# Performance work log

Hardware: AMD Instinct MI355X
Metric: run time of the kernel (lower is better)

Reference implementation:

```python
import jax, jax.numpy as jnp
import numpy as np
from jax import lax

EPS = 1e-5

def conv2d(x, w, pad, dil):
    # x: NCHW, w: OIHW
    return lax.conv_general_dilated(
        x, w, window_strides=(1, 1), padding=[(pad, pad), (pad, pad)],
        rhs_dilation=(dil, dil), dimension_numbers=("NCHW", "OIHW", "NCHW"))

def batchnorm(x, gamma, beta):
    # training-mode BN: batch statistics over (N, H, W), biased variance
    m = x.mean(axis=(0, 2, 3), keepdims=True)
    v = x.var(axis=(0, 2, 3), keepdims=True)
    xh = (x - m) * lax.rsqrt(v + EPS)
    return gamma[None, :, None, None] * xh + beta[None, :, None, None]

def maxpool2(x):
    return lax.reduce_window(x, -jnp.inf, lax.max, (1, 1, 2, 2), (1, 1, 2, 2), "VALID")

def mhsa(x, wq, bq, wk, bk, wv, bv, rel_h, rel_w, heads=1):
    B, C, H, W = x.shape
    N = H * W
    d = C // heads
    q = (conv2d(x, wq, 0, 1) + bq[None, :, None, None]).reshape(B, heads, d, N)
    k = (conv2d(x, wk, 0, 1) + bk[None, :, None, None]).reshape(B, heads, d, N)
    v = (conv2d(x, wv, 0, 1) + bv[None, :, None, None]).reshape(B, heads, d, N)
    # content-content: q^T k -> [B, h, N, N]
    cc = jnp.einsum("bhdn,bhdm->bhnm", q, k)
    # content-position: (rel_h + rel_w) reshaped to [h, d, N], transposed, times q
    pos = (rel_h + rel_w).reshape(heads, d, N)  # broadcast-sum [1,h,d,1,H]+[1,h,d,W,1]
    cp = jnp.einsum("hnd,bhdm->bhnm", jnp.swapaxes(pos, 1, 2), q)
    attn = jax.nn.softmax(cc + cp, axis=-1)
    # out = v @ attn^T
    out = jnp.einsum("bhdn,bhmn->bhdm", v, attn)
    return out.reshape(B, C, H, W)


def setup_inputs() -> dict:
    key = jax.random.key(0)
    ks = jax.random.split(key, 16)
    B, in_ch, out_ch, S = 4, 128, 256, 64
    c4 = out_ch // 4  # 64 = MHSA channel dim
    w_scale = 0.05
    inp = {
        "x": jax.random.normal(ks[0], (B, in_ch, 2 * S, 2 * S), jnp.float32),
        "dc_w1": jax.random.normal(ks[1], (out_ch, in_ch, 3, 3), jnp.float32) * w_scale,
        "dc_b1": jnp.zeros((out_ch,), jnp.float32),
        "dc_g1": jnp.ones((out_ch,), jnp.float32),
        "dc_be1": jnp.zeros((out_ch,), jnp.float32),
        "dc_w2": jax.random.normal(ks[2], (out_ch, out_ch, 3, 3), jnp.float32) * w_scale,
        "dc_b2": jnp.zeros((out_ch,), jnp.float32),
        "dc_g2": jnp.ones((out_ch,), jnp.float32),
        "dc_be2": jnp.zeros((out_ch,), jnp.float32),
        "aspp1_w": jax.random.normal(ks[3], (c4, out_ch, 1, 1), jnp.float32) * w_scale,
        "aspp1_g": jnp.ones((c4,), jnp.float32),
        "aspp1_b": jnp.zeros((c4,), jnp.float32),
        "aspp2_w": jax.random.normal(ks[4], (c4, out_ch, 3, 3), jnp.float32) * w_scale,
        "aspp2_g": jnp.ones((c4,), jnp.float32),
        "aspp2_b": jnp.zeros((c4,), jnp.float32),
        "aspp3_w": jax.random.normal(ks[5], (c4, out_ch, 3, 3), jnp.float32) * w_scale,
        "aspp3_g": jnp.ones((c4,), jnp.float32),
        "aspp3_b": jnp.zeros((c4,), jnp.float32),
        "aspp4_w": jax.random.normal(ks[6], (c4, out_ch, 3, 3), jnp.float32) * w_scale,
        "aspp4_g": jnp.ones((c4,), jnp.float32),
        "aspp4_b": jnp.zeros((c4,), jnp.float32),
        "wq": jax.random.normal(ks[7], (c4, c4, 1, 1), jnp.float32) * w_scale,
        "bq": jnp.zeros((c4,), jnp.float32),
        "wk": jax.random.normal(ks[8], (c4, c4, 1, 1), jnp.float32) * w_scale,
        "bk": jnp.zeros((c4,), jnp.float32),
        "wv": jax.random.normal(ks[9], (c4, c4, 1, 1), jnp.float32) * w_scale,
        "bv": jnp.zeros((c4,), jnp.float32),
        "rel_h": jax.random.normal(ks[10], (1, 1, c4, 1, S), jnp.float32),
        "rel_w": jax.random.normal(ks[11], (1, 1, c4, S, 1), jnp.float32),
    }
    return inp


def reference(x, dc_w1, dc_b1, dc_g1, dc_be1, dc_w2, dc_b2, dc_g2, dc_be2,
              aspp1_w, aspp1_g, aspp1_b, aspp2_w, aspp2_g, aspp2_b,
              aspp3_w, aspp3_g, aspp3_b, aspp4_w, aspp4_g, aspp4_b,
              wq, bq, wk, bk, wv, bv, rel_h, rel_w):
    dilations = (1, 3, 6, 9)
    # mpconv: MaxPool2d(2) -> double_conv
    h = maxpool2(x)
    h = jax.nn.relu(batchnorm(conv2d(h, dc_w1, 1, 1) + dc_b1[None, :, None, None], dc_g1, dc_be1))
    h = jax.nn.relu(batchnorm(conv2d(h, dc_w2, 1, 1) + dc_b2[None, :, None, None], dc_g2, dc_be2))

    aspp = [(aspp1_w, aspp1_g, aspp1_b), (aspp2_w, aspp2_g, aspp2_b),
            (aspp3_w, aspp3_g, aspp3_b), (aspp4_w, aspp4_g, aspp4_b)]
    outs = []
    for (w, g, b), dil in zip(aspp, dilations):
        pad = 0 if dil == 1 else dil
        branch = jax.nn.relu(batchnorm(conv2d(h, w, pad, dil), g, b))
        outs.append(mhsa(branch, wq, bq, wk, bk, wv, bv, rel_h, rel_w))
    return jnp.concatenate(outs, axis=1)
```

## Files before the change

### kernel.cpp

```cpp
#include <hip/hip_runtime.h>
#include <math.h>

constexpr int Bn = 4;
constexpr int S  = 64;
constexpr int N  = 4096;

#define DEV static __device__ __forceinline__

typedef __attribute__((ext_vector_type(8))) short bf16x8;
typedef __attribute__((ext_vector_type(4))) float f32x4;

DEV unsigned short bfc(float x) {
  unsigned u = __float_as_uint(x);
  unsigned r = (u + 0x7FFFu + ((u >> 16) & 1u)) >> 16;
  return (unsigned short)r;
}

DEV void fma4(float4& a, float s, const float4 u) {
  a.x = fmaf(s, u.x, a.x); a.y = fmaf(s, u.y, a.y);
  a.z = fmaf(s, u.z, a.z); a.w = fmaf(s, u.w, a.w);
}

DEV void gload_lds16(const unsigned short* g, unsigned short* l) {
  __builtin_amdgcn_global_load_lds(
      (const __attribute__((address_space(1))) void*)g,
      (__attribute__((address_space(3))) void*)l, 16, 0, 0);
}

DEV unsigned cvtpk_bf16(float lo, float hi) {
  unsigned r;
  asm("v_cvt_pk_bf16_f32 %0, %1, %2" : "=v"(r) : "v"(lo), "v"(hi));
  return r;
}
DEV void pswap32(unsigned& a, unsigned& b) {
  asm("v_permlane32_swap_b32 %0, %1" : "+v"(a), "+v"(b));
}
DEV void pswap16(unsigned& a, unsigned& b) {
  asm("v_permlane16_swap_b32 %0, %1" : "+v"(a), "+v"(b));
}

__global__ __launch_bounds__(256) void wtr_all_kernel(
    const float* __restrict__ w1, const float* __restrict__ w2,
    const float* __restrict__ a0, const float* __restrict__ a1,
    const float* __restrict__ a2, const float* __restrict__ a3,
    unsigned short* __restrict__ wt1, unsigned short* __restrict__ wt2,
    unsigned short* __restrict__ wtbr) {
  const int blk = blockIdx.x;
  const float* src; unsigned short* dst; int Cin, Cout, T, base;
  if (blk < 1152)      { src = w1; dst = wt1; Cout = 256; Cin = 128; T = 9; base = 0; }
  else if (blk < 3456) { src = w2; dst = wt2; Cout = 256; Cin = 256; T = 9; base = 1152; }
  else if (blk < 3520) { src = a0; dst = wtbr + (size_t)4 * 64 * 256;
                         Cout = 64; Cin = 256; T = 1; base = 3456; }
  else if (blk < 4096) { src = a1; dst = wtbr + (size_t)1 * 9 * 64 * 256;
                         Cout = 64; Cin = 256; T = 9; base = 3520; }
  else if (blk < 4672) { src = a2; dst = wtbr + (size_t)2 * 9 * 64 * 256;
                         Cout = 64; Cin = 256; T = 9; base = 4096; }
  else                 { src = a3; dst = wtbr + (size_t)3 * 9 * 64 * 256;
                         Cout = 64; Cin = 256; T = 9; base = 4672; }
  int i = (blk - base) * 256 + threadIdx.x;
  int ci = i % Cin;
  int r  = i / Cin;
  int t  = r / Cout;
  int co = r - t * Cout;
  dst[i] = bfc(src[((size_t)co * Cin + ci) * T + t]);
}

__global__ __launch_bounds__(256) void pool_kernel(const float* __restrict__ x,
                                                   unsigned short* __restrict__ Pp1) {
  int i = blockIdx.x * 256 + threadIdx.x;
  int xg = i & 15, y = (i >> 4) & 63, c = (i >> 10) & 127, b = i >> 17;
  const float* s = x + (((size_t)(b * 128 + c) * 128) + 2 * y) * 128 + 8 * xg;
  float4 u0 = *(const float4*)(s), u1 = *(const float4*)(s + 4);
  float4 u2 = *(const float4*)(s + 128), u3 = *(const float4*)(s + 132);
  float m0 = fmaxf(fmaxf(u0.x, u0.y), fmaxf(u2.x, u2.y));
  float m1 = fmaxf(fmaxf(u0.z, u0.w), fmaxf(u2.z, u2.w));
  float m2 = fmaxf(fmaxf(u1.x, u1.y), fmaxf(u3.x, u3.y));
  float m3 = fmaxf(fmaxf(u1.z, u1.w), fmaxf(u3.z, u3.w));
  unsigned short* d = Pp1 + (((size_t)b * 66 + y + 1) * 66 + xg * 4 + 1) * 128 + c;
  d[0] = bfc(m0); d[128] = bfc(m1); d[256] = bfc(m2); d[384] = bfc(m3);
}

template <int CTOT>
__global__ __launch_bounds__(256) void dcconv_kernel(
    const unsigned short* __restrict__ in, const unsigned short* __restrict__ wt,
    float* __restrict__ out) {
  const int Wp = 66, CSEG = CTOT / 2;
  const int w = threadIdx.x >> 6, lane = threadIdx.x & 63;
  const int ln = lane & 15, quad = lane >> 4;
  const int b = blockIdx.z >> 1, h = blockIdx.z & 1, co0 = blockIdx.y * 64;
  const int n0 = blockIdx.x * 128 + w * 32;
  const unsigned short* inb = in + (size_t)b * Wp * Wp * CTOT + h * CSEG;
  const unsigned short* wth = wt + h * CSEG;
  float* outh = out + (size_t)h * 4 * 256 * N;
  size_t pix[2];
#pragma unroll
  for (int j = 0; j < 2; j++) {
    int n = n0 + j * 16 + ln;
    int y = n >> 6, x = n & 63;
    pix[j] = ((size_t)y * Wp + x) * CTOT;
  }
  f32x4 acc[4][2];
#pragma unroll
  for (int i = 0; i < 4; i++)
#pragma unroll
    for (int j = 0; j < 2; j++) acc[i][j] = (f32x4)(0.f);
#pragma unroll
  for (int ky = 0; ky < 3; ky++)
#pragma unroll
    for (int kx = 0; kx < 3; kx++) {
      const size_t toff = ((size_t)ky * Wp + kx) * CTOT;
      const unsigned short* wtap = wth + (size_t)(ky * 3 + kx) * 256 * CTOT;
      for (int kc = 0; kc < CSEG / 32; kc++) {
        const int ko = kc * 32 + quad * 8;
        bf16x8 a[4], bb[2];
#pragma unroll
        for (int i = 0; i < 4; i++)
          a[i] = *(const bf16x8*)(wtap + (size_t)(co0 + i * 16 + ln) * CTOT + ko);
#pragma unroll
        for (int j = 0; j < 2; j++)
          bb[j] = *(const bf16x8*)(inb + pix[j] + toff + ko);
#pragma unroll
        for (int i = 0; i < 4; i++)
#pragma unroll
          for (int j = 0; j < 2; j++)
            acc[i][j] = __builtin_amdgcn_mfma_f32_16x16x32_bf16(a[i], bb[j], acc[i][j], 0, 0, 0);
      }
    }
#pragma unroll
  for (int i = 0; i < 4; i++)
#pragma unroll
    for (int j = 0; j < 2; j++)
#pragma unroll
      for (int r = 0; r < 4; r++)
        outh[((size_t)(b * 256 + co0 + i * 16 + quad * 4 + r)) * N + n0 + j * 16 + ln] =
            acc[i][j][r];
}

__global__ __launch_bounds__(256) void branch_kernel(
    const unsigned short* __restrict__ in, const unsigned short* __restrict__ wtall,
    float* __restrict__ br) {
  const int Wp = 82, halo = 9, CIN = 256;
  const int w = threadIdx.x >> 6, lane = threadIdx.x & 63;
  const int ln = lane & 15, quad = lane >> 4;
  const int bb = blockIdx.y;
  const int kbr = bb >> 2, b = bb & 3;
  const int dil = (kbr == 0) ? 1 : 3 * kbr;
  const int klo = (kbr == 0) ? 1 : 0, khi = (kbr == 0) ? 2 : 3;
  const int hd = halo - dil;
  const int cw = (w & 1) * 32, nw = (w >> 1) * 32;
  const int n0 = blockIdx.x * 64 + nw;
  const unsigned short* inb = in + (size_t)b * Wp * Wp * CIN;
  size_t pix[2];
#pragma unroll
  for (int j = 0; j < 2; j++) {
    int n = n0 + j * 16 + ln;
    int y = n >> 6, x = n & 63;
    pix[j] = ((size_t)(y + hd) * Wp + x + hd) * CIN;
  }
  f32x4 acc[2][2];
#pragma unroll
  for (int i = 0; i < 2; i++)
#pragma unroll
    for (int j = 0; j < 2; j++) acc[i][j] = (f32x4)(0.f);
  for (int ky = klo; ky < khi; ky++)
    for (int kx = klo; kx < khi; kx++) {
      const size_t toff = ((size_t)ky * Wp + kx) * dil * CIN;
      const unsigned short* wtap =
          wtall + ((size_t)kbr * 9 + ky * 3 + kx) * 64 * CIN;
      for (int kc = 0; kc < CIN / 32; kc++) {
        const int ko = kc * 32 + quad * 8;
        bf16x8 a[2], bv[2];
#pragma unroll
        for (int i = 0; i < 2; i++)
          a[i] = *(const bf16x8*)(wtap + (size_t)(cw + i * 16 + ln) * CIN + ko);
#pragma unroll
        for (int j = 0; j < 2; j++)
          bv[j] = *(const bf16x8*)(inb + pix[j] + toff + ko);
#pragma unroll
        for (int i = 0; i < 2; i++)
#pragma unroll
          for (int j = 0; j < 2; j++)
            acc[i][j] = __builtin_amdgcn_mfma_f32_16x16x32_bf16(a[i], bv[j], acc[i][j], 0, 0, 0);
      }
    }
#pragma unroll
  for (int i = 0; i < 2; i++)
#pragma unroll
    for (int j = 0; j < 2; j++)
#pragma unroll
      for (int r = 0; r < 4; r++)
        br[((size_t)bb * 64 + cw + i * 16 + quad * 4 + r) * N + n0 + j * 16 + ln] =
            acc[i][j][r];
}

__global__ __launch_bounds__(256) void bn_stats_all_kernel(
    const float* __restrict__ br,
    const float* __restrict__ g0, const float* __restrict__ b0,
    const float* __restrict__ g1, const float* __restrict__ b1,
    const float* __restrict__ g2, const float* __restrict__ b2,
    const float* __restrict__ g3, const float* __restrict__ b3,
    float* __restrict__ sta) {
  const int kbr = blockIdx.x >> 6, c = blockIdx.x & 63;
  const float* gamma = kbr == 0 ? g0 : (kbr == 1 ? g1 : (kbr == 2 ? g2 : g3));
  const float* beta  = kbr == 0 ? b0 : (kbr == 1 ? b1 : (kbr == 2 ? b2 : b3));
  const float* t = br + (size_t)kbr * 1048576;
  float* ss = sta + kbr * 128;
  float s = 0.f, s2 = 0.f;
  for (int b = 0; b < Bn; b++) {
    const float* p = t + ((size_t)(b * 64 + c)) * N;
    for (int i = threadIdx.x; i < N / 4; i += 256) {
      float4 v = *(const float4*)(p + (size_t)i * 4);
      s += (v.x + v.y) + (v.z + v.w);
      s2 = fmaf(v.x, v.x, s2); s2 = fmaf(v.y, v.y, s2);
      s2 = fmaf(v.z, v.z, s2); s2 = fmaf(v.w, v.w, s2);
    }
  }
  for (int off = 32; off; off >>= 1) {
    s += __shfl_down(s, off, 64);
    s2 += __shfl_down(s2, off, 64);
  }
  __shared__ float rs[4], rs2[4];
  const int wid = threadIdx.x >> 6, lane = threadIdx.x & 63;
  if (lane == 0) { rs[wid] = s; rs2[wid] = s2; }
  __syncthreads();
  if (threadIdx.x == 0) {
    float S1 = rs[0] + rs[1] + rs[2] + rs[3];
    float S2 = rs2[0] + rs2[1] + rs2[2] + rs2[3];
    const float cnt = (float)(Bn * N);
    float mean = S1 / cnt;
    float var = S2 / cnt - mean * mean;
    float sc = gamma[c] * rsqrtf(var + 1e-5f);
    ss[2 * c] = sc;
    ss[2 * c + 1] = beta[c] - mean * sc;
  }
}

__global__ __launch_bounds__(256) void bn_stats2_kernel(
    const float* __restrict__ ta, const float* __restrict__ tb,
    const float* __restrict__ gamma, const float* __restrict__ beta,
    float* __restrict__ ss, int C) {
  const int c = blockIdx.x;
  float s = 0.f, s2 = 0.f;
  for (int b = 0; b < Bn; b++) {
    const size_t base = ((size_t)(b * C + c)) * N;
    for (int i = threadIdx.x; i < N / 4; i += 256) {
      float4 va = *(const float4*)(ta + base + (size_t)i * 4);
      float4 vb = *(const float4*)(tb + base + (size_t)i * 4);
      float v0 = va.x + vb.x, v1 = va.y + vb.y;
      float v2 = va.z + vb.z, v3 = va.w + vb.w;
      s += (v0 + v1) + (v2 + v3);
      s2 = fmaf(v0, v0, s2); s2 = fmaf(v1, v1, s2);
      s2 = fmaf(v2, v2, s2); s2 = fmaf(v3, v3, s2);
    }
  }
  for (int off = 32; off; off >>= 1) {
    s += __shfl_down(s, off, 64);
    s2 += __shfl_down(s2, off, 64);
  }
  __shared__ float rs[4], rs2[4];
  const int wid = threadIdx.x >> 6, lane = threadIdx.x & 63;
  if (lane == 0) { rs[wid] = s; rs2[wid] = s2; }
  __syncthreads();
  if (threadIdx.x == 0) {
    float S1 = rs[0] + rs[1] + rs[2] + rs[3];
    float S2 = rs2[0] + rs2[1] + rs2[2] + rs2[3];
    const float cnt = (float)(Bn * N);
    float mean = S1 / cnt;
    float var = S2 / cnt - mean * mean;
    float sc = gamma[c] * rsqrtf(var + 1e-5f);
    ss[2 * c] = sc;
    ss[2 * c + 1] = beta[c] - mean * sc;
  }
}

__global__ __launch_bounds__(256) void bn_norm_pad2_kernel(
    const float* __restrict__ ta, const float* __restrict__ tb,
    const float* __restrict__ ss, unsigned short* __restrict__ outp,
    int Wp, int halo) {
  int i = blockIdx.x * 256 + threadIdx.x;
  int n = i & 4095, cg = (i >> 12) & 63, b = i >> 18;
  int c0 = cg * 4;
  ushort4 pk;
  float v0, v1, v2, v3;
  {
    size_t i0 = ((size_t)(b * 256 + c0 + 0)) * N + n;
    size_t i1 = i0 + N, i2 = i1 + N, i3 = i2 + N;
    v0 = fmaxf(fmaf(ta[i0] + tb[i0], ss[2 * (c0 + 0)], ss[2 * (c0 + 0) + 1]), 0.f);
    v1 = fmaxf(fmaf(ta[i1] + tb[i1], ss[2 * (c0 + 1)], ss[2 * (c0 + 1) + 1]), 0.f);
    v2 = fmaxf(fmaf(ta[i2] + tb[i2], ss[2 * (c0 + 2)], ss[2 * (c0 + 2) + 1]), 0.f);
    v3 = fmaxf(fmaf(ta[i3] + tb[i3], ss[2 * (c0 + 3)], ss[2 * (c0 + 3) + 1]), 0.f);
  }
  pk.x = bfc(v0); pk.y = bfc(v1); pk.z = bfc(v2); pk.w = bfc(v3);
  int y = n >> 6, x = n & 63;
  *(ushort4*)(outp + (((size_t)b * Wp + y + halo) * Wp + x + halo) * 256 + c0) = pk;
}

__global__ __launch_bounds__(256) void qkv_kernel(
    const float* __restrict__ br, const float* __restrict__ sta,
    const float* __restrict__ wq, const float* __restrict__ bq,
    const float* __restrict__ wk, const float* __restrict__ bk,
    const float* __restrict__ wv, const float* __restrict__ bvb,
    unsigned short* __restrict__ qTo, unsigned short* __restrict__ kTo,
    unsigned short* __restrict__ vbo) {
  const int bb = blockIdx.z;
  const int p = blockIdx.y >> 2, dg = blockIdx.y & 3;
  const float* w  = p == 0 ? wq : (p == 1 ? wk : wv);
  const float* bi = p == 0 ? bq : (p == 1 ? bk : bvb);
  __shared__ float wl[64 * 16];
  __shared__ float ssl[128];
  const int d0b = dg * 16;
  if (threadIdx.x < 128) ssl[threadIdx.x] = sta[(bb >> 2) * 128 + threadIdx.x];
  for (int i = threadIdx.x; i < 64 * 16; i += 256)
    wl[i] = w[(size_t)(d0b + (i & 15)) * 64 + (i >> 4)];
  __syncthreads();
  const int tn = threadIdx.x & 63, td = threadIdx.x >> 6;
  const int n0 = blockIdx.x * 256 + tn * 4;
  const int d0 = d0b + td * 4;
  const float* inb = br + (size_t)bb * 64 * N;
  float4 acc[4];
#pragma unroll
  for (int j = 0; j < 4; j++) {
    float bvv = bi[d0 + j];
    acc[j] = make_float4(bvv, bvv, bvv, bvv);
  }
  for (int ci = 0; ci < 64; ci++) {
    float4 u = *(const float4*)(inb + (size_t)ci * N + n0);
    const float sc = ssl[2 * ci], of = ssl[2 * ci + 1];
    u.x = fmaxf(fmaf(u.x, sc, of), 0.f);
    u.y = fmaxf(fmaf(u.y, sc, of), 0.f);
    u.z = fmaxf(fmaf(u.z, sc, of), 0.f);
    u.w = fmaxf(fmaf(u.w, sc, of), 0.f);
    float4 wv4 = *(const float4*)(wl + ci * 16 + td * 4);
    fma4(acc[0], wv4.x, u); fma4(acc[1], wv4.y, u);
    fma4(acc[2], wv4.z, u); fma4(acc[3], wv4.w, u);
  }
  const size_t slab = (size_t)bb * N * 64;
  if (p < 2) {
    unsigned short* o = (p == 0 ? qTo : kTo) + slab;
#pragma unroll
    for (int nn = 0; nn < 4; nn++) {
      ushort4 pk;
      pk.x = bfc(((const float*)&acc[0])[nn]);
      pk.y = bfc(((const float*)&acc[1])[nn]);
      pk.z = bfc(((const float*)&acc[2])[nn]);
      pk.w = bfc(((const float*)&acc[3])[nn]);
      *(ushort4*)(o + (size_t)(n0 + nn) * 64 + d0) = pk;
    }
  } else {
    unsigned short* o = vbo + slab;
#pragma unroll
    for (int j = 0; j < 4; j++) {
      ushort4 pk;
      pk.x = bfc(acc[j].x); pk.y = bfc(acc[j].y);
      pk.z = bfc(acc[j].z); pk.w = bfc(acc[j].w);
      *(ushort4*)(o + (size_t)(d0 + j) * N + n0) = pk;
    }
  }
}

__global__ __launch_bounds__(256) void posT_kernel(
    const float* __restrict__ rel_h, const float* __restrict__ rel_w,
    unsigned short* __restrict__ posT) {
  int i = blockIdx.x * 256 + threadIdx.x;
  int n = i >> 4, dq = (i & 15) * 4;
  int h = n >> 6, wc = n & 63;
  ushort4 pk;
  pk.x = bfc(rel_w[(dq + 0) * 64 + h] + rel_h[(dq + 0) * 64 + wc]);
  pk.y = bfc(rel_w[(dq + 1) * 64 + h] + rel_h[(dq + 1) * 64 + wc]);
  pk.z = bfc(rel_w[(dq + 2) * 64 + h] + rel_h[(dq + 2) * 64 + wc]);
  pk.w = bfc(rel_w[(dq + 3) * 64 + h] + rel_h[(dq + 3) * 64 + wc]);
  *(ushort4*)(posT + (size_t)n * 64 + dq) = pk;
}

__global__ __launch_bounds__(256, 3) void flash3_kernel(
    const unsigned short* __restrict__ qT, const unsigned short* __restrict__ kT,
    const unsigned short* __restrict__ posT, const unsigned short* __restrict__ vb,
    float* __restrict__ o_part, float* __restrict__ ml) {
  const int lin = blockIdx.x;
  const int xcd = lin & 7, slot = lin >> 3;
  const int bb = xcd * 2 + (slot & 1);
  const int rest = slot >> 1;
  const int mtile = rest & 31, split = rest >> 5;
  const size_t slab = (size_t)bb * N * 64;
  const unsigned short* qTs = qT + slab;
  const unsigned short* kTs = kT + slab;
  const unsigned short* vbs = vb + slab;
  const int w = threadIdx.x >> 6, lane = threadIdx.x & 63;
  const int ln = lane & 15, quad = lane >> 4;
  const int m0 = mtile * 128 + w * 32;
  __shared__ __align__(16) unsigned short As[2][4][64][32];

  const unsigned short* ssrc = (w < 2) ? kTs : qTs;
  const int rsub = lane >> 2;
  const int csw  = (lane & 3) ^ ((lane >> 3) & 3);
  const int ksub = (w & 1) * 32 + csw * 8;
  auto stage = [&](int c0, int bufi) {
#pragma unroll
    for (int j = 0; j < 4; j++)
      gload_lds16(ssrc + (size_t)(c0 + j * 16 + rsub) * 64 + ksub,
                  &As[bufi][w][j * 16][0]);
  };

  bf16x8 bq[4][2];
#pragma unroll
  for (int s = 0; s < 4; s++) {
    const unsigned short* src = (s < 2) ? qTs : posT;
#pragma unroll
    for (int mf = 0; mf < 2; mf++)
      bq[s][mf] = *(const bf16x8*)(src + (size_t)(m0 + mf * 16 + ln) * 64 +
                                   (s & 1) * 32 + quad * 8);
  }

  float m_run[2] = {-3.0e38f, -3.0e38f}, l_run[2] = {0.f, 0.f};
  f32x4 o_acc[4][2];
#pragma unroll
  for (int dt = 0; dt < 4; dt++)
#pragma unroll
    for (int mf = 0; mf < 2; mf++) o_acc[dt][mf] = (f32x4)(0.f);

  const int qsw = (quad ^ ((ln >> 1) & 3)) * 8;
  const int cbeg = split * 1024;
  stage(cbeg, 0);
  for (int t = 0; t < 16; t++) {
    const int c0 = cbeg + t * 64;
    const int buf = t & 1;
    __syncthreads();
    if (t < 15) stage(c0 + 64, buf ^ 1);
    f32x4 st[4][2];
#pragma unroll
    for (int jt = 0; jt < 4; jt++)
#pragma unroll
      for (int mf = 0; mf < 2; mf++) st[jt][mf] = (f32x4)(0.f);
    __builtin_amdgcn_s_setprio(1);
#pragma unroll
    for (int s = 0; s < 4; s++) {
#pragma unroll
      for (int jt = 0; jt < 4; jt++) {
        bf16x8 a = *(const bf16x8*)(&As[buf][s][jt * 16 + ln][qsw]);
#pragma unroll
        for (int mf = 0; mf < 2; mf++)
          st[jt][mf] = __builtin_amdgcn_mfma_f32_16x16x32_bf16(a, bq[s][mf], st[jt][mf], 0, 0, 0);
      }
    }
    __builtin_amdgcn_s_setprio(0);
    bf16x8 av[2][4];
#pragma unroll
    for (int tt = 0; tt < 2; tt++)
#pragma unroll
      for (int dt = 0; dt < 4; dt++)
        av[tt][dt] = *(const bf16x8*)(vbs + (size_t)(dt * 16 + ln) * N + c0 + tt * 32 + quad * 8);
    unsigned P0[2][4], P1[2][4];
#pragma unroll
    for (int mf = 0; mf < 2; mf++) {
      float mj[4];
#pragma unroll
      for (int jt = 0; jt < 4; jt++)
        mj[jt] = fmaxf(fmaxf(st[jt][mf][0], st[jt][mf][1]),
                       fmaxf(st[jt][mf][2], st[jt][mf][3]));
      float mx = fmaxf(fmaxf(mj[0], mj[1]), fmaxf(mj[2], mj[3]));
      mx = fmaxf(mx, __shfl_xor(mx, 16, 64));
      mx = fmaxf(mx, __shfl_xor(mx, 32, 64));
      if (!__all(mx <= m_run[mf])) {
        const float m_new = fmaxf(m_run[mf], mx);
        const float alpha = __expf(m_run[mf] - m_new);
        l_run[mf] *= alpha;
#pragma unroll
        for (int dt = 0; dt < 4; dt++)
#pragma unroll
          for (int r = 0; r < 4; r++) o_acc[dt][mf][r] *= alpha;
        m_run[mf] = m_new;
      }
      const float mc = m_run[mf];
      float psum = 0.f;
#pragma unroll
      for (int jt = 0; jt < 4; jt++) {
        float e0 = __expf(st[jt][mf][0] - mc);
        float e1 = __expf(st[jt][mf][1] - mc);
        float e2 = __expf(st[jt][mf][2] - mc);
        float e3 = __expf(st[jt][mf][3] - mc);
        psum += (e0 + e1) + (e2 + e3);
        P0[mf][jt] = cvtpk_bf16(e0, e1);
        P1[mf][jt] = cvtpk_bf16(e2, e3);
      }
      psum += __shfl_xor(psum, 16, 64);
      psum += __shfl_xor(psum, 32, 64);
      l_run[mf] += psum;
    }
    __builtin_amdgcn_s_setprio(1);
#pragma unroll
    for (int tt = 0; tt < 2; tt++) {
#pragma unroll
      for (int mf = 0; mf < 2; mf++) {
        unsigned x0 = P0[mf][2 * tt], y0 = P0[mf][2 * tt + 1];
        pswap32(x0, y0); pswap16(x0, y0);
        unsigned x1 = P1[mf][2 * tt], y1 = P1[mf][2 * tt + 1];
        pswap32(x1, y1); pswap16(x1, y1);
        union { unsigned u[4]; bf16x8 v; } bp;
        bp.u[0] = x0; bp.u[1] = x1; bp.u[2] = y0; bp.u[3] = y1;
#pragma unroll
        for (int dt = 0; dt < 4; dt++)
          o_acc[dt][mf] = __builtin_amdgcn_mfma_f32_16x16x32_bf16(av[tt][dt], bp.v, o_acc[dt][mf], 0, 0, 0);
      }
    }
    __builtin_amdgcn_s_setprio(0);
  }
  float* ob = o_part + ((size_t)(split * 16 + bb) * 64) * N;
#pragma unroll
  for (int dt = 0; dt < 4; dt++)
#pragma unroll
    for (int mf = 0; mf < 2; mf++)
#pragma unroll
      for (int r = 0; r < 4; r++) {
        int d = dt * 16 + quad * 4 + r;
        ob[(size_t)d * N + m0 + mf * 16 + ln] = o_acc[dt][mf][r];
      }
  if (quad == 0) {
#pragma unroll
    for (int mf = 0; mf < 2; mf++) {
      int m = m0 + mf * 16 + ln;
      ml[((size_t)(split * 16 + bb) * 2 + 0) * N + m] = m_run[mf];
      ml[((size_t)(split * 16 + bb) * 2 + 1) * N + m] = l_run[mf];
    }
  }
}

__global__ __launch_bounds__(256) void wcomb_kernel(const float* __restrict__ ml,
                                                    float* __restrict__ wcb) {
  int i = blockIdx.x * 256 + threadIdx.x;
  int m = i & 4095, bb = i >> 12;
  float mv[4], lv[4];
#pragma unroll
  for (int s = 0; s < 4; s++) {
    mv[s] = ml[((size_t)(s * 16 + bb) * 2 + 0) * N + m];
    lv[s] = ml[((size_t)(s * 16 + bb) * 2 + 1) * N + m];
  }
  float M = fmaxf(fmaxf(mv[0], mv[1]), fmaxf(mv[2], mv[3]));
  float wsc[4], denom = 0.f;
#pragma unroll
  for (int s = 0; s < 4; s++) {
    wsc[s] = __expf(mv[s] - M);
    denom = fmaf(wsc[s], lv[s], denom);
  }
  float inv = 1.0f / denom;
#pragma unroll
  for (int s = 0; s < 4; s++)
    wcb[(size_t)(s * 16 + bb) * N + m] = wsc[s] * inv;
}

__global__ __launch_bounds__(256) void comb_kernel(const float* __restrict__ o_part,
                                                   const float* __restrict__ wcb,
                                                   float* __restrict__ out) {
  int i = blockIdx.x * 256 + threadIdx.x;
  int m4 = i & 1023, d = (i >> 10) & 63, bb = i >> 16;
  int kbr = bb >> 2, b = bb & 3;
  float4 acc = make_float4(0.f, 0.f, 0.f, 0.f);
#pragma unroll
  for (int s = 0; s < 4; s++) {
    const float4 o = *(const float4*)(o_part + ((size_t)(s * 16 + bb) * 64 + d) * N + m4 * 4);
    const float4 wv = *(const float4*)(wcb + (size_t)(s * 16 + bb) * N + m4 * 4);
    acc.x = fmaf(o.x, wv.x, acc.x); acc.y = fmaf(o.y, wv.y, acc.y);
    acc.z = fmaf(o.z, wv.z, acc.z); acc.w = fmaf(o.w, wv.w, acc.w);
  }
  *(float4*)(out + ((size_t)(b * 256 + kbr * 64 + d)) * N + m4 * 4) = acc;
}

extern "C" void kernel_launch(void* const* d_in, const int* in_sizes, int n_in,
                              void* d_out, int out_size, void* d_ws, size_t ws_size,
                              hipStream_t stream) {
  const float* x      = (const float*)d_in[0];
  const float* dc_w1  = (const float*)d_in[1];
  const float* dc_g1  = (const float*)d_in[3];
  const float* dc_be1 = (const float*)d_in[4];
  const float* dc_w2  = (const float*)d_in[5];
  const float* dc_g2  = (const float*)d_in[7];
  const float* dc_be2 = (const float*)d_in[8];
  const float* aspp_w[4] = {(const float*)d_in[9],  (const float*)d_in[12],
                            (const float*)d_in[15], (const float*)d_in[18]};
  const float* aspp_g[4] = {(const float*)d_in[10], (const float*)d_in[13],
                            (const float*)d_in[16], (const float*)d_in[19]};
  const float* aspp_b[4] = {(const float*)d_in[11], (const float*)d_in[14],
                            (const float*)d_in[17], (const float*)d_in[20]};
  const float* wq = (const float*)d_in[21];
  const float* bq = (const float*)d_in[22];
  const float* wk = (const float*)d_in[23];
  const float* bk = (const float*)d_in[24];
  const float* wv = (const float*)d_in[25];
  const float* bv = (const float*)d_in[26];
  const float* rel_h = (const float*)d_in[27];
  const float* rel_w = (const float*)d_in[28];
  float* out = (float*)d_out;

  float* ws = (float*)d_ws;
  size_t off = 0;
  auto alloc = [&](size_t nf) { float* p = ws + off; off += nf; return p; };
  unsigned short* Pp1 = (unsigned short*)alloc((size_t)4 * 66 * 66 * 128 / 2 + 64);
  unsigned short* Pp2 = (unsigned short*)alloc((size_t)4 * 66 * 66 * 256 / 2 + 64);
  unsigned short* Pp3 = (unsigned short*)alloc((size_t)4 * 82 * 82 * 256 / 2 + 64);
  const size_t HALF = (size_t)4 * 256 * N;
  float* t1   = alloc(2 * HALF);
  float* br   = alloc((size_t)4 * 4 * 64 * N);
  float* st1  = alloc(512);
  float* st2  = alloc(512);
  float* sta  = alloc(512);
  unsigned short* qT    = (unsigned short*)alloc((size_t)16 * N * 64 / 2);
  unsigned short* kT    = (unsigned short*)alloc((size_t)16 * N * 64 / 2);
  unsigned short* vb    = (unsigned short*)alloc((size_t)16 * N * 64 / 2);
  unsigned short* posT  = (unsigned short*)alloc((size_t)N * 64 / 2);
  unsigned short* wt1   = (unsigned short*)alloc((size_t)9 * 256 * 128 / 2);
  unsigned short* wt2   = (unsigned short*)alloc((size_t)9 * 256 * 256 / 2);
  unsigned short* wtbr  = (unsigned short*)alloc((size_t)4 * 9 * 64 * 256 / 2);
  float* o_part = alloc((size_t)4 * 16 * 64 * N);
  float* mlb    = alloc((size_t)4 * 16 * 2 * N);
  float* wcb    = alloc((size_t)4 * 16 * N);

  hipMemsetAsync(Pp1, 0, (size_t)4 * 66 * 66 * 128 * 2, stream);
  hipMemsetAsync(Pp2, 0, (size_t)4 * 66 * 66 * 256 * 2, stream);
  hipMemsetAsync(Pp3, 0, (size_t)4 * 82 * 82 * 256 * 2, stream);
  hipMemsetAsync(wtbr, 0, (size_t)4 * 9 * 64 * 256 * 2, stream);

  wtr_all_kernel<<<5248, 256, 0, stream>>>(dc_w1, dc_w2, aspp_w[0], aspp_w[1],
                                           aspp_w[2], aspp_w[3], wt1, wt2, wtbr);

  pool_kernel<<<2048, 256, 0, stream>>>(x, Pp1);

  dcconv_kernel<128><<<dim3(32, 4, 8), 256, 0, stream>>>(Pp1, wt1, t1);
  bn_stats2_kernel<<<256, 256, 0, stream>>>(t1, t1 + HALF, dc_g1, dc_be1, st1, 256);
  bn_norm_pad2_kernel<<<4096, 256, 0, stream>>>(t1, t1 + HALF, st1, Pp2, 66, 1);
  dcconv_kernel<256><<<dim3(32, 4, 8), 256, 0, stream>>>(Pp2, wt2, t1);
  bn_stats2_kernel<<<256, 256, 0, stream>>>(t1, t1 + HALF, dc_g2, dc_be2, st2, 256);
  bn_norm_pad2_kernel<<<4096, 256, 0, stream>>>(t1, t1 + HALF, st2, Pp3, 82, 9);

  branch_kernel<<<dim3(64, 16), 256, 0, stream>>>(Pp3, wtbr, br);
  bn_stats_all_kernel<<<256, 256, 0, stream>>>(
      br, aspp_g[0], aspp_b[0], aspp_g[1], aspp_b[1],
      aspp_g[2], aspp_b[2], aspp_g[3], aspp_b[3], sta);

  qkv_kernel<<<dim3(16, 12, 16), 256, 0, stream>>>(br, sta, wq, bq, wk, bk,
                                                   wv, bv, qT, kT, vb);
  posT_kernel<<<256, 256, 0, stream>>>(rel_h, rel_w, posT);

  flash3_kernel<<<dim3(2048), 256, 0, stream>>>(qT, kT, posT, vb, o_part, mlb);
  wcomb_kernel<<<256, 256, 0, stream>>>(mlb, wcb);
  comb_kernel<<<4096, 256, 0, stream>>>(o_part, wcb, out);
}
```

Measured before the change: 653.9 us.

## Drop split-K in double conv, fuse QKV projections, fold softmax merge weights into combine

The double-conv kernel no longer splits the input channels into two halves writing separate partial outputs. Each block now covers 32 output channels over the full reduction, so the BN stats and normalize kernels read one tensor instead of summing two. The QKV kernel computes Q, K and V in one pass, sharing the normalized input loads. The split-softmax weight computation is folded into the combine kernel, removing a launch and an intermediate buffer. The trade-off is fewer MFMA tiles per wave in the conv and more registers in the fused QKV kernel.

```diff
diff --git a/kernel.cpp b/kernel.cpp
--- a/kernel.cpp
+++ b/kernel.cpp
@@ -84,14 +84,12 @@
 __global__ __launch_bounds__(256) void dcconv_kernel(
     const unsigned short* __restrict__ in, const unsigned short* __restrict__ wt,
     float* __restrict__ out) {
-  const int Wp = 66, CSEG = CTOT / 2;
+  const int Wp = 66;
   const int w = threadIdx.x >> 6, lane = threadIdx.x & 63;
   const int ln = lane & 15, quad = lane >> 4;
-  const int b = blockIdx.z >> 1, h = blockIdx.z & 1, co0 = blockIdx.y * 64;
+  const int b = blockIdx.z, co0 = blockIdx.y * 32;
   const int n0 = blockIdx.x * 128 + w * 32;
-  const unsigned short* inb = in + (size_t)b * Wp * Wp * CTOT + h * CSEG;
-  const unsigned short* wth = wt + h * CSEG;
-  float* outh = out + (size_t)h * 4 * 256 * N;
+  const unsigned short* inb = in + (size_t)b * Wp * Wp * CTOT;
   size_t pix[2];
 #pragma unroll
   for (int j = 0; j < 2; j++) {
@@ -99,9 +97,9 @@
     int y = n >> 6, x = n & 63;
     pix[j] = ((size_t)y * Wp + x) * CTOT;
   }
-  f32x4 acc[4][2];
-#pragma unroll
-  for (int i = 0; i < 4; i++)
+  f32x4 acc[2][2];
+#pragma unroll
+  for (int i = 0; i < 2; i++)
 #pragma unroll
     for (int j = 0; j < 2; j++) acc[i][j] = (f32x4)(0.f);
 #pragma unroll
@@ -109,30 +107,30 @@
 #pragma unroll
     for (int kx = 0; kx < 3; kx++) {
       const size_t toff = ((size_t)ky * Wp + kx) * CTOT;
-      const unsigned short* wtap = wth + (size_t)(ky * 3 + kx) * 256 * CTOT;
-      for (int kc = 0; kc < CSEG / 32; kc++) {
+      const unsigned short* wtap = wt + (size_t)(ky * 3 + kx) * 256 * CTOT;
+      for (int kc = 0; kc < CTOT / 32; kc++) {
         const int ko = kc * 32 + quad * 8;
-        bf16x8 a[4], bb[2];
-#pragma unroll
-        for (int i = 0; i < 4; i++)
+        bf16x8 a[2], bb[2];
+#pragma unroll
+        for (int i = 0; i < 2; i++)
           a[i] = *(const bf16x8*)(wtap + (size_t)(co0 + i * 16 + ln) * CTOT + ko);
 #pragma unroll
         for (int j = 0; j < 2; j++)
           bb[j] = *(const bf16x8*)(inb + pix[j] + toff + ko);
 #pragma unroll
-        for (int i = 0; i < 4; i++)
+        for (int i = 0; i < 2; i++)
 #pragma unroll
           for (int j = 0; j < 2; j++)
             acc[i][j] = __builtin_amdgcn_mfma_f32_16x16x32_bf16(a[i], bb[j], acc[i][j], 0, 0, 0);
       }
     }
 #pragma unroll
-  for (int i = 0; i < 4; i++)
+  for (int i = 0; i < 2; i++)
 #pragma unroll
     for (int j = 0; j < 2; j++)
 #pragma unroll
       for (int r = 0; r < 4; r++)
-        outh[((size_t)(b * 256 + co0 + i * 16 + quad * 4 + r)) * N + n0 + j * 16 + ln] =
+        out[((size_t)(b * 256 + co0 + i * 16 + quad * 4 + r)) * N + n0 + j * 16 + ln] =
             acc[i][j][r];
 }
 
@@ -235,22 +233,18 @@
   }
 }
 
-__global__ __launch_bounds__(256) void bn_stats2_kernel(
-    const float* __restrict__ ta, const float* __restrict__ tb,
-    const float* __restrict__ gamma, const float* __restrict__ beta,
-    float* __restrict__ ss, int C) {
+__global__ __launch_bounds__(256) void bn_stats_dc_kernel(
+    const float* __restrict__ t, const float* __restrict__ gamma,
+    const float* __restrict__ beta, float* __restrict__ ss) {
   const int c = blockIdx.x;
   float s = 0.f, s2 = 0.f;
   for (int b = 0; b < Bn; b++) {
-    const size_t base = ((size_t)(b * C + c)) * N;
+    const float* p = t + ((size_t)(b * 256 + c)) * N;
     for (int i = threadIdx.x; i < N / 4; i += 256) {
-      float4 va = *(const float4*)(ta + base + (size_t)i * 4);
-      float4 vb = *(const float4*)(tb + base + (size_t)i * 4);
-      float v0 = va.x + vb.x, v1 = va.y + vb.y;
-      float v2 = va.z + vb.z, v3 = va.w + vb.w;
-      s += (v0 + v1) + (v2 + v3);
-      s2 = fmaf(v0, v0, s2); s2 = fmaf(v1, v1, s2);
-      s2 = fmaf(v2, v2, s2); s2 = fmaf(v3, v3, s2);
+      float4 v = *(const float4*)(p + (size_t)i * 4);
+      s += (v.x + v.y) + (v.z + v.w);
+      s2 = fmaf(v.x, v.x, s2); s2 = fmaf(v.y, v.y, s2);
+      s2 = fmaf(v.z, v.z, s2); s2 = fmaf(v.w, v.w, s2);
     }
   }
   for (int off = 32; off; off >>= 1) {
@@ -273,10 +267,9 @@
   }
 }
 
-__global__ __launch_bounds__(256) void bn_norm_pad2_kernel(
-    const float* __restrict__ ta, const float* __restrict__ tb,
-    const float* __restrict__ ss, unsigned short* __restrict__ outp,
-    int Wp, int halo) {
+__global__ __launch_bounds__(256) void bn_norm_pad_kernel(
+    const float* __restrict__ ta, const float* __restrict__ ss,
+    unsigned short* __restrict__ outp, int Wp, int halo) {
   int i = blockIdx.x * 256 + threadIdx.x;
   int n = i & 4095, cg = (i >> 12) & 63, b = i >> 18;
   int c0 = cg * 4;
@@ -285,10 +278,10 @@
   {
     size_t i0 = ((size_t)(b * 256 + c0 + 0)) * N + n;
     size_t i1 = i0 + N, i2 = i1 + N, i3 = i2 + N;
-    v0 = fmaxf(fmaf(ta[i0] + tb[i0], ss[2 * (c0 + 0)], ss[2 * (c0 + 0) + 1]), 0.f);
-    v1 = fmaxf(fmaf(ta[i1] + tb[i1], ss[2 * (c0 + 1)], ss[2 * (c0 + 1) + 1]), 0.f);
-    v2 = fmaxf(fmaf(ta[i2] + tb[i2], ss[2 * (c0 + 2)], ss[2 * (c0 + 2) + 1]), 0.f);
-    v3 = fmaxf(fmaf(ta[i3] + tb[i3], ss[2 * (c0 + 3)], ss[2 * (c0 + 3) + 1]), 0.f);
+    v0 = fmaxf(fmaf(ta[i0], ss[2 * (c0 + 0)], ss[2 * (c0 + 0) + 1]), 0.f);
+    v1 = fmaxf(fmaf(ta[i1], ss[2 * (c0 + 1)], ss[2 * (c0 + 1) + 1]), 0.f);
+    v2 = fmaxf(fmaf(ta[i2], ss[2 * (c0 + 2)], ss[2 * (c0 + 2) + 1]), 0.f);
+    v3 = fmaxf(fmaf(ta[i3], ss[2 * (c0 + 3)], ss[2 * (c0 + 3) + 1]), 0.f);
   }
   pk.x = bfc(v0); pk.y = bfc(v1); pk.z = bfc(v2); pk.w = bfc(v3);
   int y = n >> 6, x = n & 63;
@@ -302,26 +295,29 @@
     const float* __restrict__ wv, const float* __restrict__ bvb,
     unsigned short* __restrict__ qTo, unsigned short* __restrict__ kTo,
     unsigned short* __restrict__ vbo) {
-  const int bb = blockIdx.z;
-  const int p = blockIdx.y >> 2, dg = blockIdx.y & 3;
-  const float* w  = p == 0 ? wq : (p == 1 ? wk : wv);
-  const float* bi = p == 0 ? bq : (p == 1 ? bk : bvb);
-  __shared__ float wl[64 * 16];
+  const int bb = blockIdx.z, dg = blockIdx.y;
+  __shared__ float wl[3][64 * 16];
   __shared__ float ssl[128];
   const int d0b = dg * 16;
   if (threadIdx.x < 128) ssl[threadIdx.x] = sta[(bb >> 2) * 128 + threadIdx.x];
-  for (int i = threadIdx.x; i < 64 * 16; i += 256)
-    wl[i] = w[(size_t)(d0b + (i & 15)) * 64 + (i >> 4)];
+  for (int i = threadIdx.x; i < 64 * 16; i += 256) {
+    const size_t widx = (size_t)(d0b + (i & 15)) * 64 + (i >> 4);
+    wl[0][i] = wq[widx];
+    wl[1][i] = wk[widx];
+    wl[2][i] = wv[widx];
+  }
   __syncthreads();
   const int tn = threadIdx.x & 63, td = threadIdx.x >> 6;
   const int n0 = blockIdx.x * 256 + tn * 4;
   const int d0 = d0b + td * 4;
   const float* inb = br + (size_t)bb * 64 * N;
-  float4 acc[4];
+  float4 acc[3][4];
 #pragma unroll
   for (int j = 0; j < 4; j++) {
-    float bvv = bi[d0 + j];
-    acc[j] = make_float4(bvv, bvv, bvv, bvv);
+    float bq_ = bq[d0 + j], bk_ = bk[d0 + j], bv_ = bvb[d0 + j];
+    acc[0][j] = make_float4(bq_, bq_, bq_, bq_);
+    acc[1][j] = make_float4(bk_, bk_, bk_, bk_);
+    acc[2][j] = make_float4(bv_, bv_, bv_, bv_);
   }
   for (int ci = 0; ci < 64; ci++) {
     float4 u = *(const float4*)(inb + (size_t)ci * N + n0);
@@ -330,29 +326,34 @@
     u.y = fmaxf(fmaf(u.y, sc, of), 0.f);
     u.z = fmaxf(fmaf(u.z, sc, of), 0.f);
     u.w = fmaxf(fmaf(u.w, sc, of), 0.f);
-    float4 wv4 = *(const float4*)(wl + ci * 16 + td * 4);
-    fma4(acc[0], wv4.x, u); fma4(acc[1], wv4.y, u);
-    fma4(acc[2], wv4.z, u); fma4(acc[3], wv4.w, u);
+#pragma unroll
+    for (int p = 0; p < 3; p++) {
+      float4 wv4 = *(const float4*)(&wl[p][ci * 16 + td * 4]);
+      fma4(acc[p][0], wv4.x, u); fma4(acc[p][1], wv4.y, u);
+      fma4(acc[p][2], wv4.z, u); fma4(acc[p][3], wv4.w, u);
+    }
   }
   const size_t slab = (size_t)bb * N * 64;
-  if (p < 2) {
+#pragma unroll
+  for (int p = 0; p < 2; p++) {
     unsigned short* o = (p == 0 ? qTo : kTo) + slab;
 #pragma unroll
     for (int nn = 0; nn < 4; nn++) {
       ushort4 pk;
-      pk.x = bfc(((const float*)&acc[0])[nn]);
-      pk.y = bfc(((const float*)&acc[1])[nn]);
-      pk.z = bfc(((const float*)&acc[2])[nn]);
-      pk.w = bfc(((const float*)&acc[3])[nn]);
+      pk.x = bfc(((const float*)&acc[p][0])[nn]);
+      pk.y = bfc(((const float*)&acc[p][1])[nn]);
+      pk.z = bfc(((const float*)&acc[p][2])[nn]);
+      pk.w = bfc(((const float*)&acc[p][3])[nn]);
       *(ushort4*)(o + (size_t)(n0 + nn) * 64 + d0) = pk;
     }
-  } else {
+  }
+  {
     unsigned short* o = vbo + slab;
 #pragma unroll
     for (int j = 0; j < 4; j++) {
       ushort4 pk;
-      pk.x = bfc(acc[j].x); pk.y = bfc(acc[j].y);
-      pk.z = bfc(acc[j].z); pk.w = bfc(acc[j].w);
+      pk.x = bfc(acc[2][j].x); pk.y = bfc(acc[2][j].y);
+      pk.z = bfc(acc[2][j].z); pk.w = bfc(acc[2][j].w);
       *(ushort4*)(o + (size_t)(d0 + j) * N + n0) = pk;
     }
   }
@@ -524,42 +525,40 @@
   }
 }
 
-__global__ __launch_bounds__(256) void wcomb_kernel(const float* __restrict__ ml,
-                                                    float* __restrict__ wcb) {
-  int i = blockIdx.x * 256 + threadIdx.x;
-  int m = i & 4095, bb = i >> 12;
-  float mv[4], lv[4];
-#pragma unroll
-  for (int s = 0; s < 4; s++) {
-    mv[s] = ml[((size_t)(s * 16 + bb) * 2 + 0) * N + m];
-    lv[s] = ml[((size_t)(s * 16 + bb) * 2 + 1) * N + m];
-  }
-  float M = fmaxf(fmaxf(mv[0], mv[1]), fmaxf(mv[2], mv[3]));
-  float wsc[4], denom = 0.f;
-#pragma unroll
-  for (int s = 0; s < 4; s++) {
-    wsc[s] = __expf(mv[s] - M);
-    denom = fmaf(wsc[s], lv[s], denom);
-  }
-  float inv = 1.0f / denom;
-#pragma unroll
-  for (int s = 0; s < 4; s++)
-    wcb[(size_t)(s * 16 + bb) * N + m] = wsc[s] * inv;
-}
-
 __global__ __launch_bounds__(256) void comb_kernel(const float* __restrict__ o_part,
-                                                   const float* __restrict__ wcb,
+                                                   const float* __restrict__ ml,
                                                    float* __restrict__ out) {
   int i = blockIdx.x * 256 + threadIdx.x;
   int m4 = i & 1023, d = (i >> 10) & 63, bb = i >> 16;
   int kbr = bb >> 2, b = bb & 3;
+  float mvv[4][4], lvv[4][4];
+#pragma unroll
+  for (int s = 0; s < 4; s++) {
+    float4 t0 = *(const float4*)(ml + ((size_t)(s * 16 + bb) * 2 + 0) * N + m4 * 4);
+    float4 t1 = *(const float4*)(ml + ((size_t)(s * 16 + bb) * 2 + 1) * N + m4 * 4);
+    mvv[s][0] = t0.x; mvv[s][1] = t0.y; mvv[s][2] = t0.z; mvv[s][3] = t0.w;
+    lvv[s][0] = t1.x; lvv[s][1] = t1.y; lvv[s][2] = t1.z; lvv[s][3] = t1.w;
+  }
+  float w4[4][4];
+#pragma unroll
+  for (int mm = 0; mm < 4; mm++) {
+    float M = fmaxf(fmaxf(mvv[0][mm], mvv[1][mm]), fmaxf(mvv[2][mm], mvv[3][mm]));
+    float wsc[4], denom = 0.f;
+#pragma unroll
+    for (int s = 0; s < 4; s++) {
+      wsc[s] = __expf(mvv[s][mm] - M);
+      denom = fmaf(wsc[s], lvv[s][mm], denom);
+    }
+    float inv = 1.0f / denom;
+#pragma unroll
+    for (int s = 0; s < 4; s++) w4[s][mm] = wsc[s] * inv;
+  }
   float4 acc = make_float4(0.f, 0.f, 0.f, 0.f);
 #pragma unroll
   for (int s = 0; s < 4; s++) {
     const float4 o = *(const float4*)(o_part + ((size_t)(s * 16 + bb) * 64 + d) * N + m4 * 4);
-    const float4 wv = *(const float4*)(wcb + (size_t)(s * 16 + bb) * N + m4 * 4);
-    acc.x = fmaf(o.x, wv.x, acc.x); acc.y = fmaf(o.y, wv.y, acc.y);
-    acc.z = fmaf(o.z, wv.z, acc.z); acc.w = fmaf(o.w, wv.w, acc.w);
+    acc.x = fmaf(o.x, w4[s][0], acc.x); acc.y = fmaf(o.y, w4[s][1], acc.y);
+    acc.z = fmaf(o.z, w4[s][2], acc.z); acc.w = fmaf(o.w, w4[s][3], acc.w);
   }
   *(float4*)(out + ((size_t)(b * 256 + kbr * 64 + d)) * N + m4 * 4) = acc;
 }
@@ -597,7 +596,7 @@
   unsigned short* Pp2 = (unsigned short*)alloc((size_t)4 * 66 * 66 * 256 / 2 + 64);
   unsigned short* Pp3 = (unsigned short*)alloc((size_t)4 * 82 * 82 * 256 / 2 + 64);
   const size_t HALF = (size_t)4 * 256 * N;
-  float* t1   = alloc(2 * HALF);
+  float* t1   = alloc(HALF);
   float* br   = alloc((size_t)4 * 4 * 64 * N);
   float* st1  = alloc(512);
   float* st2  = alloc(512);
@@ -611,7 +610,6 @@
   unsigned short* wtbr  = (unsigned short*)alloc((size_t)4 * 9 * 64 * 256 / 2);
   float* o_part = alloc((size_t)4 * 16 * 64 * N);
   float* mlb    = alloc((size_t)4 * 16 * 2 * N);
-  float* wcb    = alloc((size_t)4 * 16 * N);
 
   hipMemsetAsync(Pp1, 0, (size_t)4 * 66 * 66 * 128 * 2, stream);
   hipMemsetAsync(Pp2, 0, (size_t)4 * 66 * 66 * 256 * 2, stream);
@@ -623,23 +621,22 @@
 
   pool_kernel<<<2048, 256, 0, stream>>>(x, Pp1);
 
-  dcconv_kernel<128><<<dim3(32, 4, 8), 256, 0, stream>>>(Pp1, wt1, t1);
-  bn_stats2_kernel<<<256, 256, 0, stream>>>(t1, t1 + HALF, dc_g1, dc_be1, st1, 256);
-  bn_norm_pad2_kernel<<<4096, 256, 0, stream>>>(t1, t1 + HALF, st1, Pp2, 66, 1);
-  dcconv_kernel<256><<<dim3(32, 4, 8), 256, 0, stream>>>(Pp2, wt2, t1);
-  bn_stats2_kernel<<<256, 256, 0, stream>>>(t1, t1 + HALF, dc_g2, dc_be2, st2, 256);
-  bn_norm_pad2_kernel<<<4096, 256, 0, stream>>>(t1, t1 + HALF, st2, Pp3, 82, 9);
+  dcconv_kernel<128><<<dim3(32, 8, 4), 256, 0, stream>>>(Pp1, wt1, t1);
+  bn_stats_dc_kernel<<<256, 256, 0, stream>>>(t1, dc_g1, dc_be1, st1);
+  bn_norm_pad_kernel<<<4096, 256, 0, stream>>>(t1, st1, Pp2, 66, 1);
+  dcconv_kernel<256><<<dim3(32, 8, 4), 256, 0, stream>>>(Pp2, wt2, t1);
+  bn_stats_dc_kernel<<<256, 256, 0, stream>>>(t1, dc_g2, dc_be2, st2);
+  bn_norm_pad_kernel<<<4096, 256, 0, stream>>>(t1, st2, Pp3, 82, 9);
 
   branch_kernel<<<dim3(64, 16), 256, 0, stream>>>(Pp3, wtbr, br);
   bn_stats_all_kernel<<<256, 256, 0, stream>>>(
       br, aspp_g[0], aspp_b[0], aspp_g[1], aspp_b[1],
       aspp_g[2], aspp_b[2], aspp_g[3], aspp_b[3], sta);
 
-  qkv_kernel<<<dim3(16, 12, 16), 256, 0, stream>>>(br, sta, wq, bq, wk, bk,
-                                                   wv, bv, qT, kT, vb);
+  qkv_kernel<<<dim3(16, 4, 16), 256, 0, stream>>>(br, sta, wq, bq, wk, bk,
+                                                  wv, bv, qT, kT, vb);
   posT_kernel<<<256, 256, 0, stream>>>(rel_h, rel_w, posT);
 
   flash3_kernel<<<dim3(2048), 256, 0, stream>>>(qT, kT, posT, vb, o_part, mlb);
-  wcomb_kernel<<<256, 256, 0, stream>>>(mlb, wcb);
-  comb_kernel<<<4096, 256, 0, stream>>>(o_part, wcb, out);
-}
+  comb_kernel<<<4096, 256, 0, stream>>>(o_part, mlb, out);
+}
```

Result: slower. 693.3 us (+6.0%).
